# Performance work log

Measured on AMD Instinct MI355X. Metric: run time of the kernel, lower is better.

The kernel has to match this reference:

```python
import jax, jax.numpy as jnp
import numpy as np

EPSILON = 1e-06


def setup_inputs() -> dict:
    key = jax.random.key(0)
    k1, k2 = jax.random.split(key)
    logits = jax.random.normal(k1, (16, 2, 1024, 1024), dtype=jnp.float32)
    labels = jax.random.randint(k2, (16, 1, 1024, 1024), 0, 2, dtype=jnp.int32)
    return {"logits": logits, "labels": labels}


def reference(logits, labels):
    # Build one-hot targets: channel 0 = background (label==0), channel 1 = foreground.
    t = labels.astype(bool)                      # [B,1,H,W]
    targets = jnp.concatenate([jnp.logical_not(t), t], axis=1).astype(jnp.float32)  # [B,2,H,W]
    probs = jax.nn.softmax(logits, axis=1)       # softmax over class channel
    axes = tuple(range(2, logits.ndim))          # spatial axes (2,3)
    numerator = 2.0 * jnp.sum(targets * probs, axis=axes)               # [B,2]
    denominator = jnp.sum(probs * probs + targets * targets, axis=axes)  # [B,2]
    return 1.0 - jnp.mean(numerator / (denominator + EPSILON))
```

## Files before the change

kernel.cpp:

```cpp
#include <hip/hip_runtime.h>

constexpr int HW = 1024 * 1024;
constexpr int NB = 16;
constexpr float EPS = 1e-6f;
constexpr int BLOCKS_PER_BATCH = 128;
constexpr int THREADS = 256;
constexpr int NVEC    = HW / 4;
constexpr int TPB     = BLOCKS_PER_BATCH * THREADS;
constexpr int U       = NVEC / TPB;
constexpr int NBLK    = NB * BLOCKS_PER_BATCH;

typedef float f32x4 __attribute__((ext_vector_type(4)));
typedef int   i32x4 __attribute__((ext_vector_type(4)));

__global__ __launch_bounds__(THREADS, 8) void dice_partial(
        const float* __restrict__ logits,
        const int*   __restrict__ labels,
        f32x4*       __restrict__ ws4) {
    const int b   = blockIdx.x >> 7;
    const int blk = blockIdx.x & 127;

    const f32x4* __restrict__ L0 = reinterpret_cast<const f32x4*>(logits + (size_t)b * 2 * HW);
    const f32x4* __restrict__ L1 = reinterpret_cast<const f32x4*>(logits + (size_t)b * 2 * HW + HW);
    const i32x4* __restrict__ LB = reinterpret_cast<const i32x4*>(labels + (size_t)b * HW);

    const int base = blk * THREADS + threadIdx.x;

    f32x4 a[2], c[2];
    i32x4 t[2];
    a[0] = __builtin_nontemporal_load(&L0[base]);
    c[0] = __builtin_nontemporal_load(&L1[base]);
    t[0] = __builtin_nontemporal_load(&LB[base]);
    a[1] = __builtin_nontemporal_load(&L0[base + TPB]);
    c[1] = __builtin_nontemporal_load(&L1[base + TPB]);
    t[1] = __builtin_nontemporal_load(&LB[base + TPB]);

    float sp = 0.f, spp = 0.f, st = 0.f, stp = 0.f;

    #pragma unroll
    for (int u = 0; u < U; ++u) {
        const int cur = u & 1;
        f32x4 an, cn;
        i32x4 tn;
        const bool pf = (u + 2 < U);
        if (pf) {
            const int i = base + (u + 2) * TPB;
            an = __builtin_nontemporal_load(&L0[i]);
            cn = __builtin_nontemporal_load(&L1[i]);
            tn = __builtin_nontemporal_load(&LB[i]);
        }
        #pragma unroll
        for (int k = 0; k < 4; ++k) {
            const float p  = 1.f / (1.f + __expf(a[cur][k] - c[cur][k]));
            const float tf = (float)t[cur][k];
            sp += p; spp = fmaf(p, p, spp); st += tf; stp = fmaf(tf, p, stp);
        }
        if (pf) { a[cur] = an; c[cur] = cn; t[cur] = tn; }
    }

    #pragma unroll
    for (int off = 32; off > 0; off >>= 1) {
        sp  += __shfl_down(sp,  off);
        spp += __shfl_down(spp, off);
        st  += __shfl_down(st,  off);
        stp += __shfl_down(stp, off);
    }

    __shared__ float red[4][4];
    const int wave = threadIdx.x >> 6;
    const int lane = threadIdx.x & 63;
    if (lane == 0) {
        red[wave][0] = sp; red[wave][1] = spp; red[wave][2] = st; red[wave][3] = stp;
    }
    __syncthreads();
    if (threadIdx.x == 0) {
        f32x4 r;
        r.x = red[0][0] + red[1][0] + red[2][0] + red[3][0];
        r.y = red[0][1] + red[1][1] + red[2][1] + red[3][1];
        r.z = red[0][2] + red[1][2] + red[2][2] + red[3][2];
        r.w = red[0][3] + red[1][3] + red[2][3] + red[3][3];
        ws4[blockIdx.x] = r;
    }
}

__global__ __launch_bounds__(1024) void dice_reduce(
        const f32x4* __restrict__ ws4,
        float*       __restrict__ out) {
    const int wave = threadIdx.x >> 6;
    const int lane = threadIdx.x & 63;

    f32x4 v = ws4[wave * BLOCKS_PER_BATCH + lane]
            + ws4[wave * BLOCKS_PER_BATCH + 64 + lane];

    #pragma unroll
    for (int off = 32; off > 0; off >>= 1) {
        v.x += __shfl_down(v.x, off);
        v.y += __shfl_down(v.y, off);
        v.z += __shfl_down(v.z, off);
        v.w += __shfl_down(v.w, off);
    }

    __shared__ float terms[NB];
    if (lane == 0) {
        const float Sp  = v.x;
        const float Spp = v.y;
        const float St  = v.z;
        const float Stp = v.w;
        const float N = (float)HW;

        const float num1 = 2.f * Stp;
        const float den1 = Spp + St;
        const float num0 = 2.f * (N - St - Sp + Stp);
        const float den0 = (N - 2.f * Sp + Spp) + (N - St);

        terms[wave] = num0 / (den0 + EPS) + num1 / (den1 + EPS);
    }
    __syncthreads();
    if (threadIdx.x == 0) {
        float s = 0.f;
        #pragma unroll
        for (int i = 0; i < NB; ++i) s += terms[i];
        out[0] = 1.f - s / 32.f;
    }
}

extern "C" void kernel_launch(void* const* d_in, const int* in_sizes, int n_in,
                              void* d_out, int out_size, void* d_ws, size_t ws_size,
                              hipStream_t stream) {
    const float* logits = (const float*)d_in[0];
    const int*   labels = (const int*)d_in[1];
    float* out = (float*)d_out;
    f32x4* ws4 = (f32x4*)d_ws;

    dice_partial<<<NBLK, THREADS, 0, stream>>>(logits, labels, ws4);
    dice_reduce<<<1, 1024, 0, stream>>>(ws4, out);
}
```

Measured before the change: 218.3 us.

## Double blocks per batch and issue all loads upfront before compute

Doubles the grid to 256 blocks per batch, so each thread now handles 4 vector iterations instead of 8. All 12 vector loads are issued up front behind a scheduling barrier, replacing the rolling two-deep prefetch, to maximise memory-level parallelism per wave. The occupancy hint drops from 8 to 6 to leave room for the extra registers. The final reduction is updated to sum 256 partials per batch. The trade-off is higher register pressure and more partial results to reduce.

```diff
diff --git a/kernel.cpp b/kernel.cpp
--- a/kernel.cpp
+++ b/kernel.cpp
@@ -3,7 +3,7 @@
 constexpr int HW = 1024 * 1024;
 constexpr int NB = 16;
 constexpr float EPS = 1e-6f;
-constexpr int BLOCKS_PER_BATCH = 128;
+constexpr int BLOCKS_PER_BATCH = 256;
 constexpr int THREADS = 256;
 constexpr int NVEC    = HW / 4;
 constexpr int TPB     = BLOCKS_PER_BATCH * THREADS;
@@ -13,12 +13,12 @@
 typedef float f32x4 __attribute__((ext_vector_type(4)));
 typedef int   i32x4 __attribute__((ext_vector_type(4)));
 
-__global__ __launch_bounds__(THREADS, 8) void dice_partial(
+__global__ __launch_bounds__(THREADS, 6) void dice_partial(
         const float* __restrict__ logits,
         const int*   __restrict__ labels,
         f32x4*       __restrict__ ws4) {
-    const int b   = blockIdx.x >> 7;
-    const int blk = blockIdx.x & 127;
+    const int b   = blockIdx.x >> 8;
+    const int blk = blockIdx.x & 255;
 
     const f32x4* __restrict__ L0 = reinterpret_cast<const f32x4*>(logits + (size_t)b * 2 * HW);
     const f32x4* __restrict__ L1 = reinterpret_cast<const f32x4*>(logits + (size_t)b * 2 * HW + HW);
@@ -26,37 +26,35 @@
 
     const int base = blk * THREADS + threadIdx.x;
 
-    f32x4 a[2], c[2];
-    i32x4 t[2];
-    a[0] = __builtin_nontemporal_load(&L0[base]);
-    c[0] = __builtin_nontemporal_load(&L1[base]);
-    t[0] = __builtin_nontemporal_load(&LB[base]);
-    a[1] = __builtin_nontemporal_load(&L0[base + TPB]);
-    c[1] = __builtin_nontemporal_load(&L1[base + TPB]);
-    t[1] = __builtin_nontemporal_load(&LB[base + TPB]);
+    f32x4 a0 = __builtin_nontemporal_load(&L0[base + 0 * TPB]);
+    f32x4 c0 = __builtin_nontemporal_load(&L1[base + 0 * TPB]);
+    i32x4 t0 = __builtin_nontemporal_load(&LB[base + 0 * TPB]);
+    f32x4 a1 = __builtin_nontemporal_load(&L0[base + 1 * TPB]);
+    f32x4 c1 = __builtin_nontemporal_load(&L1[base + 1 * TPB]);
+    i32x4 t1 = __builtin_nontemporal_load(&LB[base + 1 * TPB]);
+    f32x4 a2 = __builtin_nontemporal_load(&L0[base + 2 * TPB]);
+    f32x4 c2 = __builtin_nontemporal_load(&L1[base + 2 * TPB]);
+    i32x4 t2 = __builtin_nontemporal_load(&LB[base + 2 * TPB]);
+    f32x4 a3 = __builtin_nontemporal_load(&L0[base + 3 * TPB]);
+    f32x4 c3 = __builtin_nontemporal_load(&L1[base + 3 * TPB]);
+    i32x4 t3 = __builtin_nontemporal_load(&LB[base + 3 * TPB]);
+    __builtin_amdgcn_sched_barrier(0);
 
     float sp = 0.f, spp = 0.f, st = 0.f, stp = 0.f;
 
-    #pragma unroll
-    for (int u = 0; u < U; ++u) {
-        const int cur = u & 1;
-        f32x4 an, cn;
-        i32x4 tn;
-        const bool pf = (u + 2 < U);
-        if (pf) {
-            const int i = base + (u + 2) * TPB;
-            an = __builtin_nontemporal_load(&L0[i]);
-            cn = __builtin_nontemporal_load(&L1[i]);
-            tn = __builtin_nontemporal_load(&LB[i]);
+    #define CONSUME(A, C, T)                                              \
+        _Pragma("unroll")                                                 \
+        for (int k = 0; k < 4; ++k) {                                     \
+            const float p  = 1.f / (1.f + __expf((A)[k] - (C)[k]));       \
+            const float tf = (float)(T)[k];                               \
+            sp += p; spp = fmaf(p, p, spp); st += tf; stp = fmaf(tf, p, stp); \
         }
-        #pragma unroll
-        for (int k = 0; k < 4; ++k) {
-            const float p  = 1.f / (1.f + __expf(a[cur][k] - c[cur][k]));
-            const float tf = (float)t[cur][k];
-            sp += p; spp = fmaf(p, p, spp); st += tf; stp = fmaf(tf, p, stp);
-        }
-        if (pf) { a[cur] = an; c[cur] = cn; t[cur] = tn; }
-    }
+
+    CONSUME(a0, c0, t0)
+    CONSUME(a1, c1, t1)
+    CONSUME(a2, c2, t2)
+    CONSUME(a3, c3, t3)
+    #undef CONSUME
 
     #pragma unroll
     for (int off = 32; off > 0; off >>= 1) {
@@ -89,8 +87,8 @@
     const int wave = threadIdx.x >> 6;
     const int lane = threadIdx.x & 63;
 
-    f32x4 v = ws4[wave * BLOCKS_PER_BATCH + lane]
-            + ws4[wave * BLOCKS_PER_BATCH + 64 + lane];
+    const f32x4* p = ws4 + wave * BLOCKS_PER_BATCH;
+    f32x4 v = p[lane] + p[lane + 64] + p[lane + 128] + p[lane + 192];
 
     #pragma unroll
     for (int off = 32; off > 0; off >>= 1) {
```

Measured after the change: 214.7 us. No clear change (-1.6%).
